# Optimization experiments

Hardware: AMD Instinct MI355X
Metric: run time of the kernel (lower is better)

Reference implementation:

```python
import jax, jax.numpy as jnp
import numpy as np

B, D_IN, D_HID, D_OUT = 16384, 256, 512, 256
E, K = 8, 2  # expert_num, activate_num


def setup_inputs() -> dict:
    key = jax.random.key(0)
    ks = jax.random.split(key, 6)
    s_in = 1.0 / np.sqrt(D_IN)
    s_hid = 1.0 / np.sqrt(D_HID)
    return {
        "x": jax.random.normal(ks[0], (B, D_IN), dtype=jnp.float32),
        "Wg": jax.random.normal(ks[1], (D_IN, E), dtype=jnp.float32) * s_in,
        "W1": jax.random.normal(ks[2], (E, D_IN, D_HID), dtype=jnp.float32) * s_in,
        "b1": jnp.zeros((E, D_HID), dtype=jnp.float32),
        "W2": jax.random.normal(ks[3], (E, D_HID, D_OUT), dtype=jnp.float32) * s_hid,
        "b2": jnp.zeros((E, D_OUT), dtype=jnp.float32),
    }


def reference(x, Wg, W1, b1, W2, b2):
    # Gating: logits -> top-k -> softmax over the k selected logits.
    # (nn.Dropout on gate logits is identity at inference.)
    gate_logits = x @ Wg                              # [B, E]
    weights, selected = jax.lax.top_k(gate_logits, K)  # [B, K], [B, K]
    weights = jax.nn.softmax(weights.astype(jnp.float32), axis=1).astype(x.dtype)

    # Expert compute, vectorized over experts (same math as the per-expert
    # gather/compute/scatter loop; tokens not routed to expert e get weight 0).
    h = jax.nn.relu(jnp.einsum("bd,edh->ebh", x, W1) + b1[:, None, :])  # [E, B, H]
    expert_out = jnp.einsum("ebh,eho->ebo", h, W2) + b2[:, None, :]      # [E, B, O]

    # Combine weights: combine[b, e] = sum_k weights[b,k] * [selected[b,k]==e]
    one_hot = jax.nn.one_hot(selected, E, dtype=x.dtype)  # [B, K, E]
    combine = jnp.einsum("bk,bke->be", weights, one_hot)  # [B, E]
    results = jnp.einsum("be,ebo->bo", combine, expert_out)  # [B, O]
    return results
```

## Files before the change

### kernel.cpp

```cpp
#include <hip/hip_runtime.h>
#include <hip/hip_bf16.h>

typedef __bf16 bf16x8 __attribute__((ext_vector_type(8)));
typedef __bf16 bf16x4 __attribute__((ext_vector_type(4)));
typedef float f32x4 __attribute__((ext_vector_type(4)));
typedef float f32x16 __attribute__((ext_vector_type(16)));

#define NTOK 16384
#define DIN  256
#define DHID 512
#define DOUT 256
#define NEXP 8

#define MFMA32(a, b, c) __builtin_amdgcn_mfma_f32_32x32x16_bf16(a, b, c, 0, 0, 0)
#define GLD16(gp, lp)                                                       \
  __builtin_amdgcn_global_load_lds(                                         \
      (__attribute__((address_space(1))) void*)(gp),                        \
      (__attribute__((address_space(3))) void*)(lp), 16, 0, 0)

__global__ __launch_bounds__(256) void prep_kernel(
    const float* __restrict__ x, const float* __restrict__ wg,
    const float* __restrict__ w1, const float* __restrict__ w2,
    int* __restrict__ cnt, int* __restrict__ btok, float* __restrict__ bw,
    __bf16* __restrict__ xbf, __bf16* __restrict__ w1bf,
    __bf16* __restrict__ w2bf) {
  __shared__ int lcnt[NEXP];
  __shared__ int lbase[NEXP];
  const int b = blockIdx.x;
  const int tid = threadIdx.x;

  if (b >= 512) {
    if (b < 1024) {
      int e = (b - 512) >> 6;
      int flat = ((b - 512) & 63) * 256 + tid;
      int kg = flat >> 9;
      int n = flat & 511;
      const float* s = w1 + ((size_t)e * 256 + (size_t)kg * 8) * 512 + n;
      bf16x8 t;
#pragma unroll
      for (int j = 0; j < 8; ++j) t[j] = (__bf16)s[(size_t)j * 512];
      *(bf16x8*)(w1bf + (size_t)(e * 512 + n) * 256 + kg * 8) = t;
    } else {
      int e = (b - 1024) >> 6;
      int fi = ((b - 1024) & 63) * 256 + tid;
      int l31v = fi & 31;
      int hiv = (fi >> 5) & 1;
      int kwv = (fi >> 6) & 3;
      int aiv = (fi >> 8) & 1;
      int wov = (fi >> 9) & 3;
      int hcv = (fi >> 11) & 7;
      int hid0 = hcv * 64 + kwv * 16 + hiv * 8;
      int o = wov * 64 + aiv * 32 + l31v;
      const float* s = w2 + ((size_t)e * 512 + hid0) * 256 + o;
      bf16x8 t;
#pragma unroll
      for (int j = 0; j < 8; ++j) t[j] = (__bf16)s[(size_t)j * 256];
      *(bf16x8*)(w2bf + (size_t)e * 131072 + (size_t)fi * 8) = t;
    }
    return;
  }

  if (tid < NEXP) lcnt[tid] = 0;

  const int sub = tid & 7;
  const int tslot = tid >> 3;
  const int token = b * 32 + tslot;
  const f32x4* xr = (const f32x4*)(x + (size_t)token * DIN + sub * 32);
  const float* wr0 = wg + (size_t)sub * 32 * NEXP;

  bf16x8 xb[4];
  f32x4 p0 = {0.f, 0.f, 0.f, 0.f}, p1 = {0.f, 0.f, 0.f, 0.f};
#pragma unroll
  for (int j4 = 0; j4 < 8; ++j4) {
    f32x4 xv = xr[j4];
    const float* wr = wr0 + j4 * 32;
#pragma unroll
    for (int d = 0; d < 4; ++d) {
      float xs_ = xv[d];
      p0 += xs_ * *(const f32x4*)(wr + 8 * d);
      p1 += xs_ * *(const f32x4*)(wr + 8 * d + 4);
      xb[j4 >> 1][(j4 & 1) * 4 + d] = (__bf16)xs_;
    }
  }
  {
    bf16x8* xdst = (bf16x8*)(xbf + (size_t)token * DIN + sub * 32);
#pragma unroll
    for (int i = 0; i < 4; ++i) xdst[i] = xb[i];
  }

  double acc[NEXP];
#pragma unroll
  for (int d = 0; d < 4; ++d) {
    acc[d] = (double)p0[d];
    acc[4 + d] = (double)p1[d];
  }
#pragma unroll
  for (int off = 1; off < 8; off <<= 1)
#pragma unroll
    for (int e = 0; e < NEXP; ++e) acc[e] += __shfl_xor(acc[e], off, 64);

  __syncthreads();

  int i1 = 0, i2 = 0, o1 = 0, o2 = 0;
  float w1s = 0.f, w2s = 0.f;
  if (sub == 0) {
    double bv1 = acc[0];
#pragma unroll
    for (int e = 1; e < NEXP; ++e)
      if (acc[e] > bv1) { bv1 = acc[e]; i1 = e; }
    double bv2 = -1e300;
#pragma unroll
    for (int e = 0; e < NEXP; ++e)
      if (e != i1 && acc[e] > bv2) { bv2 = acc[e]; i2 = e; }
    float dd = expf((float)(bv2 - bv1));
    w1s = 1.0f / (1.0f + dd);
    w2s = dd * w1s;
    o1 = atomicAdd(&lcnt[i1], 1);
    o2 = atomicAdd(&lcnt[i2], 1);
  }
  __syncthreads();
  if (tid < NEXP) lbase[tid] = atomicAdd(&cnt[tid], lcnt[tid]);
  __syncthreads();
  if (sub == 0) {
    int s1 = lbase[i1] + o1, s2 = lbase[i2] + o2;
    btok[i1 * NTOK + s1] = token;
    bw[i1 * NTOK + s1] = w1s;
    btok[i2 * NTOK + s2] = token | 16384;
    bw[i2 * NTOK + s2] = w2s;
  }
}

__global__ __launch_bounds__(256, 2) void ffn_kernel(
    const __bf16* __restrict__ xbf, const __bf16* __restrict__ w1bf,
    const __bf16* __restrict__ w2bf, const float* __restrict__ b1g,
    const float* __restrict__ b2g, const int* __restrict__ cnt,
    const int* __restrict__ btok, const float* __restrict__ bw,
    __bf16* __restrict__ pout) {
  __shared__ __align__(16) __bf16 wb1[2][64 * 256];
  __shared__ __align__(16) __bf16 hs[64 * 64];
  __shared__ int tok[64];
  __shared__ int srow[64];
  __shared__ float wgt[64];
  __shared__ float b2s[DOUT];
  __shared__ float b1s[DHID];

  int b = blockIdx.x;
  int e = -1, start = 0;
  {
    int a0 = 0;
#pragma unroll
    for (int q = 0; q < NEXP; ++q) {
      int t = (cnt[q] + 63) >> 6;
      if (e < 0 && b < a0 + t) { e = q; start = (b - a0) * 64; }
      a0 += t;
    }
  }
  if (e < 0) return;
  const int ce = cnt[e];
  const int rot = (blockIdx.x >> 3) & 7;

  const int tid = threadIdx.x;
  if (tid < 64) {
    int idx = start + tid;
    bool v = idx < ce;
    int entry = v ? btok[e * NTOK + idx] : 0;
    int tk = entry & 16383;
    tok[tid] = tk;
    srow[tid] = (entry >> 14) * NTOK + tk;
    wgt[tid] = v ? bw[e * NTOK + idx] : 0.0f;
  }
  b2s[tid] = b2g[e * DOUT + tid];
  b1s[tid] = b1g[e * DHID + tid];
  b1s[tid + 256] = b1g[e * DHID + tid + 256];
  __syncthreads();

  const int lane = tid & 63;
  const int wid = tid >> 6;
  const int hi = lane >> 5;
  const int l31 = lane & 31;
  const int wh = wid >> 1;
  const int wt = wid & 1;
  const int wo = wid;

  bf16x8 xB[16];
  {
    const __bf16* xr = xbf + (size_t)tok[wt * 32 + l31] * DIN + hi * 8;
#pragma unroll
    for (int kw = 0; kw < 16; ++kw) xB[kw] = *(const bf16x8*)(xr + kw * 16);
  }

  const __bf16* w1e = w1bf + (size_t)e * DHID * DIN;
  const __bf16* w2e = w2bf + (size_t)e * DOUT * DHID;

  f32x16 acc[2][2];
#pragma unroll
  for (int ai = 0; ai < 2; ++ai)
#pragma unroll
    for (int bi = 0; bi < 2; ++bi)
#pragma unroll
      for (int r = 0; r < 16; ++r) acc[ai][bi][r] = 0.f;

#define STAGE_W1(bufidx, hcv)                                               \
  {                                                                         \
    _Pragma("unroll")                                                       \
    for (int j = 0; j < 8; ++j) {                                           \
      int W = wid * 8 + j;                                                  \
      int n1 = 2 * W + hi;                                                  \
      int s1 = l31 ^ (n1 & 31);                                             \
      GLD16(w1e + (size_t)((hcv) * 64 + n1) * DIN + s1 * 8,                 \
            &wb1[bufidx][W * 512]);                                         \
    }                                                                       \
  }

  STAGE_W1(0, rot);

#pragma unroll
  for (int hc0 = 0; hc0 < 8; ++hc0) {
    const int hc = (hc0 + rot) & 7;
    const int cur = hc0 & 1;

    bf16x8 wfr[8];
    {
      const __bf16* w2t = w2e + ((size_t)(hc * 4 + wo) << 12);
#pragma unroll
      for (int j = 0; j < 8; ++j)
        wfr[j] = *(const bf16x8*)(w2t + j * 512 + lane * 8);
    }
    __builtin_amdgcn_sched_barrier(0);
    if (hc0 < 7) {
      STAGE_W1(cur ^ 1, (hc0 + 1 + rot) & 7);
    }
    __builtin_amdgcn_sched_barrier(0);
    if (hc0 < 7) {
      asm volatile("s_waitcnt vmcnt(16)" ::: "memory");
    } else {
      asm volatile("s_waitcnt vmcnt(8)" ::: "memory");
    }
    __builtin_amdgcn_sched_barrier(0);
    __builtin_amdgcn_s_barrier();
    __builtin_amdgcn_sched_barrier(0);

    f32x16 Sp[2];
#pragma unroll
    for (int r = 0; r < 16; ++r) { Sp[0][r] = 0.f; Sp[1][r] = 0.f; }
#pragma unroll
    for (int kw = 0; kw < 16; ++kw) {
      int row = wh * 32 + l31;
      int s = (kw * 2 + hi) ^ (row & 31);
      bf16x8 a = *(const bf16x8*)((const char*)&wb1[cur][0] + row * 512 + s * 16);
      Sp[kw & 1] = MFMA32(a, xB[kw], Sp[kw & 1]);
    }
    f32x16 S = Sp[0] + Sp[1];
#pragma unroll
    for (int g = 0; g < 4; ++g) {
      int hl = wh * 32 + 8 * g + 4 * hi;
      f32x4 bv = *(const f32x4*)(&b1s[hc * 64 + hl]);
      bf16x4 pk;
#pragma unroll
      for (int r = 0; r < 4; ++r)
        pk[r] = (__bf16)fmaxf(S[4 * g + r] + bv[r], 0.f);
      int m = wt * 32 + l31;
      int slt = (hl >> 3) ^ (m & 7);
      *(bf16x4*)((char*)hs + m * 128 + slt * 16 + (hl & 7) * 2) = pk;
    }
    asm volatile("s_waitcnt lgkmcnt(0)" ::: "memory");
    __builtin_amdgcn_sched_barrier(0);
    __builtin_amdgcn_s_barrier();
    __builtin_amdgcn_sched_barrier(0);

#pragma unroll
    for (int kw = 0; kw < 4; ++kw) {
      bf16x8 hf[2];
#pragma unroll
      for (int bi = 0; bi < 2; ++bi) {
        int m = bi * 32 + l31;
        int s = (kw * 2 + hi) ^ (m & 7);
        hf[bi] = *(const bf16x8*)((const char*)hs + m * 128 + s * 16);
      }
      acc[0][0] = MFMA32(wfr[0 * 4 + kw], hf[0], acc[0][0]);
      acc[0][1] = MFMA32(wfr[0 * 4 + kw], hf[1], acc[0][1]);
      acc[1][0] = MFMA32(wfr[1 * 4 + kw], hf[0], acc[1][0]);
      acc[1][1] = MFMA32(wfr[1 * 4 + kw], hf[1], acc[1][1]);
    }
  }
#undef STAGE_W1

#pragma unroll
  for (int bi = 0; bi < 2; ++bi) {
    int tm = bi * 32 + l31;
    if (start + tm < ce) {
      float wv = wgt[tm];
      __bf16* prow = pout + (size_t)srow[tm] * DOUT;
#pragma unroll
      for (int ai = 0; ai < 2; ++ai) {
#pragma unroll
        for (int g = 0; g < 4; ++g) {
          int o0 = wo * 64 + ai * 32 + 8 * g + 4 * hi;
          f32x4 bv = *(const f32x4*)(&b2s[o0]);
          bf16x4 pk;
#pragma unroll
          for (int r = 0; r < 4; ++r)
            pk[r] = (__bf16)(wv * (acc[ai][bi][4 * g + r] + bv[r]));
          *(bf16x4*)(prow + o0) = pk;
        }
      }
    }
  }
}

__global__ __launch_bounds__(256) void combine_kernel(const __bf16* __restrict__ pout,
                                                      float* __restrict__ out) {
  int f = blockIdx.x * 256 + threadIdx.x;
  bf16x8 a = *(const bf16x8*)(pout + (size_t)f * 8);
  bf16x8 b = *(const bf16x8*)(pout + (size_t)NTOK * DOUT + (size_t)f * 8);
  float4 o0, o1;
  o0.x = (float)a[0] + (float)b[0];
  o0.y = (float)a[1] + (float)b[1];
  o0.z = (float)a[2] + (float)b[2];
  o0.w = (float)a[3] + (float)b[3];
  o1.x = (float)a[4] + (float)b[4];
  o1.y = (float)a[5] + (float)b[5];
  o1.z = (float)a[6] + (float)b[6];
  o1.w = (float)a[7] + (float)b[7];
  float4* dst = (float4*)(out + (size_t)f * 8);
  dst[0] = o0;
  dst[1] = o1;
}

extern "C" void kernel_launch(void* const* d_in, const int* in_sizes, int n_in,
                              void* d_out, int out_size, void* d_ws, size_t ws_size,
                              hipStream_t stream) {
  const float* x = (const float*)d_in[0];
  const float* Wg = (const float*)d_in[1];
  const float* W1 = (const float*)d_in[2];
  const float* b1 = (const float*)d_in[3];
  const float* W2 = (const float*)d_in[4];
  const float* b2 = (const float*)d_in[5];
  float* out = (float*)d_out;

  char* ws = (char*)d_ws;
  int* cnt = (int*)(ws + 0);
  int* btok = (int*)(ws + 256);
  float* bw = (float*)(ws + 524544);
  __bf16* xbf = (__bf16*)(ws + 1048832);
  __bf16* w1bf = (__bf16*)(ws + 9437440);
  __bf16* w2bf = (__bf16*)(ws + 11534592);
  __bf16* pout = (__bf16*)(ws + 13631744);

  hipMemsetAsync(cnt, 0, NEXP * sizeof(int), stream);

  prep_kernel<<<dim3(1536), dim3(256), 0, stream>>>(x, Wg, W1, W2, cnt, btok,
                                                    bw, xbf, w1bf, w2bf);
  ffn_kernel<<<dim3(520), dim3(256), 0, stream>>>(xbf, w1bf, w2bf, b1, b2,
                                                  cnt, btok, bw, pout);
  combine_kernel<<<dim3(NTOK * DOUT / 8 / 256), dim3(256), 0, stream>>>(pout, out);
}
```

Before: 157.5 us.

## Use 128-token tiles with 512 threads and fuse combine via float atomics

The FFN kernel now processes 128 routed tokens per block with 8 waves instead of 64 tokens with 4. Each wave owns a 32-column output slice, and the W2 fragments are double-buffered in registers across hidden chunks. The separate combine kernel and bf16 partial buffer are removed: results are atomically added in fp32 directly into a zeroed output, which adds a memset. This cuts launches, intermediate traffic and per-token W1 staging, at the cost of many scattered fp32 atomics.

```diff
diff --git a/kernel.cpp b/kernel.cpp
--- a/kernel.cpp
+++ b/kernel.cpp
@@ -11,6 +11,7 @@
 #define DHID 512
 #define DOUT 256
 #define NEXP 8
+#define MAXB 264
 
 #define MFMA32(a, b, c) __builtin_amdgcn_mfma_f32_32x32x16_bf16(a, b, c, 0, 0, 0)
 #define GLD16(gp, lp)                                                       \
@@ -43,14 +44,12 @@
     } else {
       int e = (b - 1024) >> 6;
       int fi = ((b - 1024) & 63) * 256 + tid;
-      int l31v = fi & 31;
-      int hiv = (fi >> 5) & 1;
-      int kwv = (fi >> 6) & 3;
-      int aiv = (fi >> 8) & 1;
-      int wov = (fi >> 9) & 3;
-      int hcv = (fi >> 11) & 7;
-      int hid0 = hcv * 64 + kwv * 16 + hiv * 8;
-      int o = wov * 64 + aiv * 32 + l31v;
+      int lane = fi & 63;
+      int kw = (fi >> 6) & 3;
+      int wo = (fi >> 8) & 7;
+      int hc = (fi >> 11) & 7;
+      int hid0 = hc * 64 + kw * 16 + (lane >> 5) * 8;
+      int o = wo * 32 + (lane & 31);
       const float* s = w2 + ((size_t)e * 512 + hid0) * 256 + o;
       bf16x8 t;
 #pragma unroll
@@ -130,19 +129,18 @@
   }
 }
 
-__global__ __launch_bounds__(256, 2) void ffn_kernel(
+__global__ __launch_bounds__(512, 2) void ffn_kernel(
     const __bf16* __restrict__ xbf, const __bf16* __restrict__ w1bf,
     const __bf16* __restrict__ w2bf, const float* __restrict__ b1g,
     const float* __restrict__ b2g, const int* __restrict__ cnt,
     const int* __restrict__ btok, const float* __restrict__ bw,
-    __bf16* __restrict__ pout) {
+    float* __restrict__ out) {
   __shared__ __align__(16) __bf16 wb1[2][64 * 256];
-  __shared__ __align__(16) __bf16 hs[64 * 64];
-  __shared__ int tok[64];
-  __shared__ int srow[64];
-  __shared__ float wgt[64];
+  __shared__ __align__(16) __bf16 hs[128 * 64];
+  __shared__ int tok[128];
+  __shared__ float wgt[128];
+  __shared__ float b1s[DHID];
   __shared__ float b2s[DOUT];
-  __shared__ float b1s[DHID];
 
   int b = blockIdx.x;
   int e = -1, start = 0;
@@ -150,8 +148,8 @@
     int a0 = 0;
 #pragma unroll
     for (int q = 0; q < NEXP; ++q) {
-      int t = (cnt[q] + 63) >> 6;
-      if (e < 0 && b < a0 + t) { e = q; start = (b - a0) * 64; }
+      int t = (cnt[q] + 127) >> 7;
+      if (e < 0 && b < a0 + t) { e = q; start = (b - a0) * 128; }
       a0 += t;
     }
   }
@@ -160,81 +158,75 @@
   const int rot = (blockIdx.x >> 3) & 7;
 
   const int tid = threadIdx.x;
-  if (tid < 64) {
+  if (tid < 128) {
     int idx = start + tid;
     bool v = idx < ce;
     int entry = v ? btok[e * NTOK + idx] : 0;
-    int tk = entry & 16383;
-    tok[tid] = tk;
-    srow[tid] = (entry >> 14) * NTOK + tk;
+    tok[tid] = entry & 16383;
     wgt[tid] = v ? bw[e * NTOK + idx] : 0.0f;
   }
-  b2s[tid] = b2g[e * DOUT + tid];
-  b1s[tid] = b1g[e * DHID + tid];
-  b1s[tid + 256] = b1g[e * DHID + tid + 256];
+  if (tid < 256) b2s[tid] = b2g[e * DOUT + tid];
+  b1s[tid & 511] = b1g[e * DHID + (tid & 511)];
   __syncthreads();
 
   const int lane = tid & 63;
   const int wid = tid >> 6;
   const int hi = lane >> 5;
   const int l31 = lane & 31;
-  const int wh = wid >> 1;
-  const int wt = wid & 1;
-  const int wo = wid;
+  const int wh = wid >> 2;
+  const int wtq = wid & 3;
 
   bf16x8 xB[16];
   {
-    const __bf16* xr = xbf + (size_t)tok[wt * 32 + l31] * DIN + hi * 8;
+    const __bf16* xr = xbf + (size_t)tok[wtq * 32 + l31] * DIN + hi * 8;
 #pragma unroll
     for (int kw = 0; kw < 16; ++kw) xB[kw] = *(const bf16x8*)(xr + kw * 16);
   }
 
   const __bf16* w1e = w1bf + (size_t)e * DHID * DIN;
-  const __bf16* w2e = w2bf + (size_t)e * DOUT * DHID;
-
-  f32x16 acc[2][2];
-#pragma unroll
-  for (int ai = 0; ai < 2; ++ai)
-#pragma unroll
-    for (int bi = 0; bi < 2; ++bi)
-#pragma unroll
-      for (int r = 0; r < 16; ++r) acc[ai][bi][r] = 0.f;
+  const __bf16* w2e = w2bf + (size_t)e * 131072;
+
+  f32x16 acc[4];
+#pragma unroll
+  for (int bi = 0; bi < 4; ++bi)
+#pragma unroll
+    for (int r = 0; r < 16; ++r) acc[bi][r] = 0.f;
 
 #define STAGE_W1(bufidx, hcv)                                               \
   {                                                                         \
     _Pragma("unroll")                                                       \
-    for (int j = 0; j < 8; ++j) {                                           \
-      int W = wid * 8 + j;                                                  \
+    for (int j = 0; j < 4; ++j) {                                           \
+      int W = wid * 4 + j;                                                  \
       int n1 = 2 * W + hi;                                                  \
       int s1 = l31 ^ (n1 & 31);                                             \
       GLD16(w1e + (size_t)((hcv) * 64 + n1) * DIN + s1 * 8,                 \
             &wb1[bufidx][W * 512]);                                         \
     }                                                                       \
   }
-
+#define LOAD_W2(slot, hcv)                                                  \
+  {                                                                         \
+    const __bf16* w2t = w2e + (size_t)(((hcv) * 8 + wid) * 4) * 512;        \
+    _Pragma("unroll")                                                       \
+    for (int kw = 0; kw < 4; ++kw)                                          \
+      wfrP[slot][kw] = *(const bf16x8*)(w2t + kw * 512 + lane * 8);         \
+  }
+
+  bf16x8 wfrP[2][4];
   STAGE_W1(0, rot);
+  LOAD_W2(0, rot);
 
 #pragma unroll
   for (int hc0 = 0; hc0 < 8; ++hc0) {
     const int hc = (hc0 + rot) & 7;
     const int cur = hc0 & 1;
 
-    bf16x8 wfr[8];
-    {
-      const __bf16* w2t = w2e + ((size_t)(hc * 4 + wo) << 12);
-#pragma unroll
-      for (int j = 0; j < 8; ++j)
-        wfr[j] = *(const bf16x8*)(w2t + j * 512 + lane * 8);
-    }
-    __builtin_amdgcn_sched_barrier(0);
     if (hc0 < 7) {
-      STAGE_W1(cur ^ 1, (hc0 + 1 + rot) & 7);
-    }
-    __builtin_amdgcn_sched_barrier(0);
-    if (hc0 < 7) {
-      asm volatile("s_waitcnt vmcnt(16)" ::: "memory");
+      const int hcn = (hc0 + 1 + rot) & 7;
+      STAGE_W1(cur ^ 1, hcn);
+      LOAD_W2(cur ^ 1, hcn);
+      asm volatile("s_waitcnt vmcnt(8)" ::: "memory");
     } else {
-      asm volatile("s_waitcnt vmcnt(8)" ::: "memory");
+      asm volatile("s_waitcnt vmcnt(0)" ::: "memory");
     }
     __builtin_amdgcn_sched_barrier(0);
     __builtin_amdgcn_s_barrier();
@@ -259,7 +251,7 @@
 #pragma unroll
       for (int r = 0; r < 4; ++r)
         pk[r] = (__bf16)fmaxf(S[4 * g + r] + bv[r], 0.f);
-      int m = wt * 32 + l31;
+      int m = wtq * 32 + l31;
       int slt = (hl >> 3) ^ (m & 7);
       *(bf16x4*)((char*)hs + m * 128 + slt * 16 + (hl & 7) * 2) = pk;
     }
@@ -270,61 +262,31 @@
 
 #pragma unroll
     for (int kw = 0; kw < 4; ++kw) {
-      bf16x8 hf[2];
-#pragma unroll
-      for (int bi = 0; bi < 2; ++bi) {
+#pragma unroll
+      for (int bi = 0; bi < 4; ++bi) {
         int m = bi * 32 + l31;
         int s = (kw * 2 + hi) ^ (m & 7);
-        hf[bi] = *(const bf16x8*)((const char*)hs + m * 128 + s * 16);
+        bf16x8 hf = *(const bf16x8*)((const char*)hs + m * 128 + s * 16);
+        acc[bi] = MFMA32(wfrP[cur][kw], hf, acc[bi]);
       }
-      acc[0][0] = MFMA32(wfr[0 * 4 + kw], hf[0], acc[0][0]);
-      acc[0][1] = MFMA32(wfr[0 * 4 + kw], hf[1], acc[0][1]);
-      acc[1][0] = MFMA32(wfr[1 * 4 + kw], hf[0], acc[1][0]);
-      acc[1][1] = MFMA32(wfr[1 * 4 + kw], hf[1], acc[1][1]);
     }
   }
 #undef STAGE_W1
-
-#pragma unroll
-  for (int bi = 0; bi < 2; ++bi) {
+#undef LOAD_W2
+
+#pragma unroll
+  for (int bi = 0; bi < 4; ++bi) {
     int tm = bi * 32 + l31;
     if (start + tm < ce) {
       float wv = wgt[tm];
-      __bf16* prow = pout + (size_t)srow[tm] * DOUT;
-#pragma unroll
-      for (int ai = 0; ai < 2; ++ai) {
-#pragma unroll
-        for (int g = 0; g < 4; ++g) {
-          int o0 = wo * 64 + ai * 32 + 8 * g + 4 * hi;
-          f32x4 bv = *(const f32x4*)(&b2s[o0]);
-          bf16x4 pk;
-#pragma unroll
-          for (int r = 0; r < 4; ++r)
-            pk[r] = (__bf16)(wv * (acc[ai][bi][4 * g + r] + bv[r]));
-          *(bf16x4*)(prow + o0) = pk;
-        }
+      float* orow = out + (size_t)tok[tm] * DOUT;
+#pragma unroll
+      for (int r = 0; r < 16; ++r) {
+        int oc = wid * 32 + (r & 3) + 8 * (r >> 2) + 4 * hi;
+        unsafeAtomicAdd(orow + oc, wv * (acc[bi][r] + b2s[oc]));
       }
     }
   }
-}
-
-__global__ __launch_bounds__(256) void combine_kernel(const __bf16* __restrict__ pout,
-                                                      float* __restrict__ out) {
-  int f = blockIdx.x * 256 + threadIdx.x;
-  bf16x8 a = *(const bf16x8*)(pout + (size_t)f * 8);
-  bf16x8 b = *(const bf16x8*)(pout + (size_t)NTOK * DOUT + (size_t)f * 8);
-  float4 o0, o1;
-  o0.x = (float)a[0] + (float)b[0];
-  o0.y = (float)a[1] + (float)b[1];
-  o0.z = (float)a[2] + (float)b[2];
-  o0.w = (float)a[3] + (float)b[3];
-  o1.x = (float)a[4] + (float)b[4];
-  o1.y = (float)a[5] + (float)b[5];
-  o1.z = (float)a[6] + (float)b[6];
-  o1.w = (float)a[7] + (float)b[7];
-  float4* dst = (float4*)(out + (size_t)f * 8);
-  dst[0] = o0;
-  dst[1] = o1;
 }
 
 extern "C" void kernel_launch(void* const* d_in, const int* in_sizes, int n_in,
@@ -345,13 +307,12 @@
   __bf16* xbf = (__bf16*)(ws + 1048832);
   __bf16* w1bf = (__bf16*)(ws + 9437440);
   __bf16* w2bf = (__bf16*)(ws + 11534592);
-  __bf16* pout = (__bf16*)(ws + 13631744);
 
   hipMemsetAsync(cnt, 0, NEXP * sizeof(int), stream);
+  hipMemsetAsync(out, 0, (size_t)NTOK * DOUT * sizeof(float), stream);
 
   prep_kernel<<<dim3(1536), dim3(256), 0, stream>>>(x, Wg, W1, W2, cnt, btok,
                                                     bw, xbf, w1bf, w2bf);
-  ffn_kernel<<<dim3(520), dim3(256), 0, stream>>>(xbf, w1bf, w2bf, b1, b2,
-                                                  cnt, btok, bw, pout);
-  combine_kernel<<<dim3(NTOK * DOUT / 8 / 256), dim3(256), 0, stream>>>(pout, out);
+  ffn_kernel<<<dim3(MAXB), dim3(512), 0, stream>>>(xbf, w1bf, w2bf, b1, b2,
+                                                   cnt, btok, bw, out);
 }
```

Result: slower. 357.8 us (+127.1%).
